# Performance work log

Measured on AMD Instinct MI355X. Metric: run time of the kernel, lower is better.

The kernel has to match this reference:

```python
import jax, jax.numpy as jnp
import numpy as np
import math

# e3nn-style fully-connected Clebsch-Gordan tensor product
# irreps_in1 = 64x0e + 64x1e + 64x2e   (dim 576)
# irreps_in2 =  1x0e +  1x1e +  1x2e   (dim 9, e.g. spherical harmonics)
# irreps_out = 64x0e + 64x1e + 64x2e   (dim 576), shared weights
MUL1, MUL2, MULO = 64, 1, 64
LS = [0, 1, 2]
N_BATCH = 32768


def _su2_cg(j1, m1, j2, m2, j3, m3):
    # SU(2) Clebsch-Gordan coefficient <j1 m1 j2 m2 | j3 m3> (Racah formula)
    if m3 != m1 + m2:
        return 0.0
    f = math.factorial
    c = (2 * j3 + 1) * f(j1 + j2 - j3) * f(j1 - j2 + j3) * f(-j1 + j2 + j3) / f(j1 + j2 + j3 + 1)
    c = math.sqrt(c)
    c *= math.sqrt(f(j3 + m3) * f(j3 - m3) * f(j1 - m1) * f(j1 + m1) * f(j2 - m2) * f(j2 + m2))
    s = 0.0
    for k in range(max(0, j2 - j3 - m1, j1 - j3 + m2), min(j1 + j2 - j3, j1 - m1, j2 + m2) + 1):
        s += (-1.0) ** k / (f(k) * f(j1 + j2 - j3 - k) * f(j1 - m1 - k) * f(j2 + m2 - k)
                            * f(j3 - j2 + m1 + k) * f(j3 - j1 - m2 + k))
    return c * s


def _q_real_to_complex(l):
    # unitary change of basis, columns = real-SH index, rows = complex m (e3nn convention)
    q = np.zeros((2 * l + 1, 2 * l + 1), dtype=np.complex128)
    r2 = 1.0 / math.sqrt(2.0)
    for m in range(-l, 0):
        q[l + m, l + abs(m)] = r2
        q[l + m, l - abs(m)] = -1j * r2
    q[l, l] = 1.0
    for m in range(1, l + 1):
        q[l + m, l + m] = (-1) ** m * r2
        q[l + m, l - m] = 1j * (-1) ** m * r2
    return (-1j) ** l * q


def _real_cg(l1, l2, l3):
    # CG tensor in the real spherical-harmonic basis, unit Frobenius norm (wigner_3j-like)
    C = np.zeros((2 * l1 + 1, 2 * l2 + 1, 2 * l3 + 1), dtype=np.complex128)
    for m1 in range(-l1, l1 + 1):
        for m2 in range(-l2, l2 + 1):
            m3 = m1 + m2
            if abs(m3) <= l3:
                C[l1 + m1, l2 + m2, l3 + m3] = _su2_cg(l1, m1, l2, m2, l3, m3)
    U1, U2, U3 = _q_real_to_complex(l1), _q_real_to_complex(l2), _q_real_to_complex(l3)
    Cr = np.einsum('ia,jb,kc,ijk->abc', U1, U2, np.conj(U3), C)
    assert np.abs(Cr.imag).max() < 1e-9, 'real-basis CG should be real'
    Cr = Cr.real
    return (Cr / np.linalg.norm(Cr)).astype(np.float32)


PATHS = [(l1, l2, l3) for l1 in LS for l2 in LS for l3 in LS if abs(l1 - l2) <= l3 <= l1 + l2]
CG = {p: jnp.asarray(_real_cg(*p)) for p in PATHS}
N_PATHS_TO = {l3: sum(1 for p in PATHS if p[2] == l3) for l3 in LS}
ALPHA = {l3: 1.0 / math.sqrt(MUL1 * MUL2 * N_PATHS_TO[l3]) for l3 in LS}  # path normalization
WEIGHT_NUMEL = len(PATHS) * MUL1 * MUL2 * MULO  # 15 * 4096 = 61440
DIM1 = MUL1 * sum(2 * l + 1 for l in LS)  # 576
DIM2 = MUL2 * sum(2 * l + 1 for l in LS)  # 9


def _split1(x):
    segs, off = [], 0
    for l in LS:
        d = MUL1 * (2 * l + 1)
        segs.append(x[:, off:off + d].reshape(-1, MUL1, 2 * l + 1))
        off += d
    return segs


def _split2(y):
    segs, off = [], 0
    for l in LS:
        d = 2 * l + 1
        segs.append(y[:, off:off + d])
        off += d
    return segs


def tensor_product(x, y, W):
    # W (x (CG-otimes) y): per-path weighted Clebsch-Gordan contraction
    xs, ys = _split1(x), _split2(y)  # xs[l]: [N,64,2l+1], ys[l]: [N,2l+1]
    N = x.shape[0]
    outs = [jnp.zeros((N, MULO, 2 * l + 1), x.dtype) for l in LS]
    off = 0
    for (l1, l2, l3) in PATHS:
        Wp = W[off:off + MUL1 * MULO].reshape(MUL1, MULO)  # [u, w] (v = 1)
        off += MUL1 * MULO
        outs[l3] = outs[l3] + ALPHA[l3] * jnp.einsum(
            'nui,nj,ijk,uw->nwk', xs[l1], ys[l2], CG[(l1, l2, l3)], Wp)
    return jnp.concatenate([o.reshape(N, -1) for o in outs], axis=-1)  # [N, 576]


def setup_inputs() -> dict:
    key = jax.random.key(0)
    kx, ky, kw = jax.random.split(key, 3)
    x = jax.random.normal(kx, (N_BATCH, DIM1), dtype=jnp.float32)
    y = jax.random.normal(ky, (N_BATCH, DIM2), dtype=jnp.float32)
    W = jax.random.normal(kw, (WEIGHT_NUMEL,), dtype=jnp.float32)
    return {'x': x, 'y': y, 'W': W}


def reference(x, y, W):
    return tensor_product(x, y, W)
```

## Files before the change

### kernel.cpp

```cpp
#include <hip/hip_runtime.h>
#include <cmath>
#include <complex>
#include <algorithm>

#define NPATH 15
constexpr int PL1[NPATH] = {0,0,0, 1,1,1,1,1,1, 2,2,2,2,2,2};
constexpr int PL2[NPATH] = {0,1,2, 0,1,1,1,2,2, 0,1,1,2,2,2};
constexpr int PL3[NPATH] = {0,1,2, 1,0,1,2,1,2, 2,1,2,0,1,2};
constexpr int CGOFF[NPATH] = {0,1,10,35,44,53,80,125,170,245,270,315,390,415,490};
constexpr int CGTOT = 615;
constexpr int YOFF[3] = {0,1,4};

constexpr int GB[8] = {0,9,24,33,48,63,88,103};
constexpr int YGTOT = 137;

struct CGArg { float v[CGTOT]; };

static double factd(int n){ double r=1.0; for(int i=2;i<=n;++i) r*=(double)i; return r; }

static double su2_cg(int j1,int m1,int j2,int m2,int j3,int m3){
  if (m3 != m1+m2) return 0.0;
  double c = (double)(2*j3+1) * factd(j1+j2-j3) * factd(j1-j2+j3) * factd(-j1+j2+j3)
             / factd(j1+j2+j3+1);
  c = std::sqrt(c);
  c *= std::sqrt(factd(j3+m3)*factd(j3-m3)*factd(j1-m1)*factd(j1+m1)*factd(j2-m2)*factd(j2+m2));
  double s = 0.0;
  int kmin = std::max(0, std::max(j2-j3-m1, j1-j3+m2));
  int kmax = std::min(j1+j2-j3, std::min(j1-m1, j2+m2));
  for (int k=kmin;k<=kmax;++k){
    double d = factd(k)*factd(j1+j2-j3-k)*factd(j1-m1-k)*factd(j2+m2-k)
             * factd(j3-j2+m1+k)*factd(j3-j1-m2+k);
    s += ((k&1)? -1.0 : 1.0)/d;
  }
  return c*s;
}

static void qmat(int l, std::complex<double>* q){
  int d = 2*l+1;
  for (int a=0;a<d*d;++a) q[a] = std::complex<double>(0.0,0.0);
  const double r2 = 1.0/std::sqrt(2.0);
  for (int m=-l; m<0; ++m){
    q[(l+m)*d + (l-m)] = std::complex<double>(r2, 0.0);
    q[(l+m)*d + (l+m)] = std::complex<double>(0.0, -r2);
  }
  q[l*d + l] = std::complex<double>(1.0,0.0);
  for (int m=1; m<=l; ++m){
    double sg = (m&1)? -1.0 : 1.0;
    q[(l+m)*d + (l+m)] = std::complex<double>(sg*r2, 0.0);
    q[(l+m)*d + (l-m)] = std::complex<double>(0.0, sg*r2);
  }
  std::complex<double> ph = (l==0)? std::complex<double>(1,0)
                        : (l==1)? std::complex<double>(0,-1)
                                : std::complex<double>(-1,0);
  for (int a=0;a<d*d;++a) q[a] *= ph;
}

static void compute_cg(float* outv){
  const int npaths_to[3] = {3,6,6};
  for (int p=0;p<NPATH;++p){
    int l1=PL1[p], l2=PL2[p], l3=PL3[p];
    int d1=2*l1+1, d2=2*l2+1, d3=2*l3+1;
    std::complex<double> C[5][5][5];
    for (int a=0;a<5;++a) for(int b=0;b<5;++b) for(int c=0;c<5;++c) C[a][b][c]=std::complex<double>(0,0);
    for (int m1=-l1;m1<=l1;++m1) for (int m2=-l2;m2<=l2;++m2){
      int m3=m1+m2;
      if (std::abs(m3)<=l3) C[l1+m1][l2+m2][l3+m3] = su2_cg(l1,m1,l2,m2,l3,m3);
    }
    std::complex<double> U1[25],U2[25],U3[25];
    qmat(l1,U1); qmat(l2,U2); qmat(l3,U3);
    double Cr[5][5][5]; double nrm=0.0;
    for (int a=0;a<d1;++a) for (int b=0;b<d2;++b) for (int c=0;c<d3;++c){
      std::complex<double> s(0,0);
      for (int i=0;i<d1;++i) for (int j=0;j<d2;++j) for (int k=0;k<d3;++k)
        s += U1[i*d1+a]*U2[j*d2+b]*std::conj(U3[k*d3+c])*C[i][j][k];
      Cr[a][b][c] = s.real();
      nrm += s.real()*s.real();
    }
    nrm = std::sqrt(nrm);
    double alpha = 1.0/std::sqrt(64.0*(double)npaths_to[l3]);
    float* o = outv + CGOFF[p];
    int idx=0;
    for (int a=0;a<d1;++a) for (int b=0;b<d2;++b) for (int c=0;c<d3;++c)
      o[idx++] = (float)(Cr[a][b][c]/nrm*alpha);
  }
}

typedef short bf16x8 __attribute__((ext_vector_type(8)));
typedef float f32x4 __attribute__((ext_vector_type(4)));

#define MFMA16(A,B,C) __builtin_amdgcn_mfma_f32_16x16x32_bf16((A),(B),(C),0,0,0)

__device__ __forceinline__ unsigned cvtpk_bf16(float a, float b){
  unsigned r;
  asm("v_cvt_pk_bf16_f32 %0, %1, %2" : "=v"(r) : "v"(a), "v"(b));
  return r;
}

__device__ __forceinline__ bf16x8 afrag(const unsigned short* s_xt, int plane, int kt, int row, int q){
  int c = (kt*4 + q) ^ (row & 7);
  return *reinterpret_cast<const bf16x8*>(s_xt + (plane*16 + row)*64 + c*8);
}
__device__ __forceinline__ bf16x8 wfrag(const unsigned short* WT, int p, int wt, int cl, int kt, int q){
  return *reinterpret_cast<const bf16x8*>(WT + p*4096 + (wt*16+cl)*64 + kt*32 + q*8);
}
__device__ __forceinline__ void xt_write_pk(unsigned short* s_xt, int plane, int n, int t16, uint2 pk){
  const int swz = (((t16>>1)^(n&7))<<3) + ((t16&1)<<2);
  *reinterpret_cast<uint2*>(s_xt + (plane*16 + n)*64 + swz) = pk;
}

__device__ __forceinline__ void pack_x(const float4& r0, const float4* r1, const float4* r2, uint2* xpk){
  const float* f0 = reinterpret_cast<const float*>(&r0);
  const float* f1 = reinterpret_cast<const float*>(r1);
  const float* f2 = reinterpret_cast<const float*>(r2);
  xpk[0].x = cvtpk_bf16(f0[0], f0[1]);  xpk[0].y = cvtpk_bf16(f0[2], f0[3]);
  #pragma unroll
  for (int i=0;i<3;++i){
    xpk[1+i].x = cvtpk_bf16(f1[0*3+i], f1[1*3+i]);
    xpk[1+i].y = cvtpk_bf16(f1[2*3+i], f1[3*3+i]);
  }
  #pragma unroll
  for (int i=0;i<5;++i){
    xpk[4+i].x = cvtpk_bf16(f2[0*5+i], f2[1*5+i]);
    xpk[4+i].y = cvtpk_bf16(f2[2*5+i], f2[3*5+i]);
  }
}

template<int G,int D1,int D3,int AB>
__device__ __forceinline__ void gen1(const bf16x8* xf, bf16x8 b0, bf16x8 b1,
                                     const float* ygc, f32x4* acc){
  const f32x4 z4 = {0.f,0.f,0.f,0.f};
  #pragma unroll
  for (int i=0;i<D1;++i){
    f32x4 T = MFMA16(b0, xf[2*i], z4);  T = MFMA16(b1, xf[2*i+1], T);
    #pragma unroll
    for (int k=0;k<D3;++k){
      float yv = ygc[(GB[G] + i*D3 + k)*16];
      acc[AB+k] += T*yv;
    }
  }
}
template<int D1,int AB>
__device__ __forceinline__ void dl0(const bf16x8* xf, bf16x8 b0, bf16x8 b1,
                                    float cy, f32x4* acc){
  const f32x4 z4 = {0.f,0.f,0.f,0.f};
  #pragma unroll
  for (int i=0;i<D1;++i){
    f32x4 T = MFMA16(b0, xf[2*i], z4);  T = MFMA16(b1, xf[2*i+1], T);
    acc[AB+i] += T*cy;
  }
}
template<int D3,int YE,int AB>
__device__ __forceinline__ void d0l(const bf16x8* xf, bf16x8 b0, bf16x8 b1,
                                    float c, const float* ygc, f32x4* acc){
  const f32x4 z4 = {0.f,0.f,0.f,0.f};
  f32x4 T = MFMA16(b0, xf[0], z4);  T = MFMA16(b1, xf[1], T);
  #pragma unroll
  for (int k=0;k<D3;++k){
    float yv = c*ygc[(YE+k)*16];
    acc[AB+k] += T*yv;
  }
}
template<int D1,int YE>
__device__ __forceinline__ void dll0(const bf16x8* xf, bf16x8 b0, bf16x8 b1,
                                     float c, const float* ygc, f32x4* acc){
  const f32x4 z4 = {0.f,0.f,0.f,0.f};
  f32x4 s = z4;
  #pragma unroll
  for (int i=0;i<D1;++i){
    f32x4 T = MFMA16(b0, xf[2*i], z4);  T = MFMA16(b1, xf[2*i+1], T);
    s += T*ygc[(YE+i)*16];
  }
  acc[0] += s*c;
}

__global__ __launch_bounds__(256, 3)
void tp_kernel(const float* __restrict__ x, const float* __restrict__ y,
               const unsigned short* __restrict__ WT, float* __restrict__ out, CGArg cga)
{
  __shared__ __align__(16) unsigned short s_xt[9*16*64];
  __shared__ __align__(16) float s_yg[YGTOT*16];

  const int bid = blockIdx.x;
  const int tile = (bid & 7) | ((bid >> 4) << 3);
  const int half = (bid >> 3) & 1;
  const int n0 = tile * 16;

  const int tid = threadIdx.x;
  const int n_s = tid>>4, t16 = tid&15;

  {
    const float* xb = x + (size_t)(n0 + n_s)*576;
    float4 r0 = *reinterpret_cast<const float4*>(xb + t16*4);
    float4 r1[3], r2[5];
    #pragma unroll
    for (int i=0;i<3;++i) r1[i] = *reinterpret_cast<const float4*>(xb + 64 + t16*12 + 4*i);
    #pragma unroll
    for (int i=0;i<5;++i) r2[i] = *reinterpret_cast<const float4*>(xb + 256 + t16*20 + 4*i);

    float yl[9];
    {
      const float* yrow = y + (size_t)(n0 + t16)*9;
      #pragma unroll
      for (int j=0;j<9;++j) yl[j] = yrow[j];
    }

    uint2 xpk[9];
    pack_x(r0, r1, r2, xpk);
    #pragma unroll
    for (int pl=0; pl<9; ++pl) xt_write_pk(s_xt, pl, n_s, t16, xpk[pl]);

    if (tid < 16){
      #pragma unroll
      for (int j=0;j<9;++j) s_yg[(128+j)*16 + tid] = yl[j];
    }

    if (half == 0){
      constexpr int GL[4] = {0,2,4,6};
      #pragma unroll
      for (int u=0; u<4; ++u){
        constexpr int GPp[4] = {5,7,10,13};
        const int p = GPp[u];
        const int d2=2*PL2[p]+1, d3=2*PL3[p]+1;
        const int cnt = (2*PL1[p]+1)*d3*16;
        for (int idx=tid; idx<cnt; idx+=256){
          int ik = idx >> 4;
          int i  = ik/d3;
          int k  = ik - i*d3;
          float s=0.f;
          for (int j=0;j<d2;++j)
            s += yl[YOFF[PL2[p]]+j]*cga.v[CGOFF[p]+(i*d2+j)*d3+k];
          s_yg[(GB[GL[u]]+ik)*16 + t16] = s;
        }
      }
    } else {
      constexpr int GL[4] = {1,3,5,7};
      #pragma unroll
      for (int u=0; u<4; ++u){
        constexpr int GPp[4] = {6,8,11,14};
        const int p = GPp[u];
        const int d2=2*PL2[p]+1, d3=2*PL3[p]+1;
        const int cnt = (2*PL1[p]+1)*d3*16;
        for (int idx=tid; idx<cnt; idx+=256){
          int ik = idx >> 4;
          int i  = ik/d3;
          int k  = ik - i*d3;
          float s=0.f;
          for (int j=0;j<d2;++j)
            s += yl[YOFF[PL2[p]]+j]*cga.v[CGOFF[p]+(i*d2+j)*d3+k];
          s_yg[(GB[GL[u]]+ik)*16 + t16] = s;
        }
      }
    }
  }
  __syncthreads();

  const int lane = tid & 63, wt = tid >> 6;
  const int cl = lane & 15, q = lane >> 4;
  const float* ygc = s_yg + cl;
  const float y0 = ygc[128*16];
  const int wbase = wt*16 + q*4;

  const f32x4 z4 = {0.f,0.f,0.f,0.f};
  bf16x8 b0,b1,nb0,nb1;

  #define LDB(P) { nb0 = wfrag(WT,P,wt,cl,0,q); nb1 = wfrag(WT,P,wt,cl,1,q); }
  #define ADV    { b0 = nb0; b1 = nb1; }

  if (half == 0){
    f32x4 acc[4] = {z4,z4,z4,z4};
    bf16x8 xf0[2];
    #pragma unroll
    for (int kt=0;kt<2;++kt) xf0[kt] = afrag(s_xt, 0, kt, cl, q);
    b0 = wfrag(WT,0,wt,cl,0,q); b1 = wfrag(WT,0,wt,cl,1,q);

    LDB(1);  dl0<1,0>(xf0, b0,b1, cga.v[CGOFF[0]]*y0, acc);              ADV;
    LDB(3);  d0l<3,129,1>(xf0, b0,b1, cga.v[CGOFF[1]], ygc, acc);        ADV;
    bf16x8 xf1[6];
    #pragma unroll
    for (int i=0;i<3;++i)
      #pragma unroll
      for (int kt=0;kt<2;++kt) xf1[2*i+kt] = afrag(s_xt, 1+i, kt, cl, q);
    LDB(4);  dl0<3,1>(xf1, b0,b1, cga.v[CGOFF[3]]*y0, acc);              ADV;
    LDB(5);  dll0<3,129>(xf1, b0,b1, cga.v[CGOFF[4]], ygc, acc);         ADV;
    LDB(7);  gen1<0,3,3,1>(xf1, b0,b1, ygc, acc);                        ADV;
    LDB(10); gen1<2,3,3,1>(xf1, b0,b1, ygc, acc);                        ADV;
    bf16x8 xf2[10];
    #pragma unroll
    for (int i=0;i<5;++i)
      #pragma unroll
      for (int kt=0;kt<2;++kt) xf2[2*i+kt] = afrag(s_xt, 4+i, kt, cl, q);
    LDB(12); gen1<4,5,3,1>(xf2, b0,b1, ygc, acc);                        ADV;
    LDB(13); dll0<5,132>(xf2, b0,b1, cga.v[CGOFF[12]], ygc, acc);        ADV;
             gen1<6,5,3,1>(xf2, b0,b1, ygc, acc);

    float* orow = out + (size_t)(n0 + cl)*576;
    *reinterpret_cast<float4*>(orow + wbase) =
        make_float4(acc[0][0],acc[0][1],acc[0][2],acc[0][3]);
    float4 v0 = make_float4(acc[1][0],acc[2][0],acc[3][0],acc[1][1]);
    float4 v1 = make_float4(acc[2][1],acc[3][1],acc[1][2],acc[2][2]);
    float4 v2 = make_float4(acc[3][2],acc[1][3],acc[2][3],acc[3][3]);
    float4* qp = reinterpret_cast<float4*>(orow + 64 + wbase*3);
    qp[0]=v0; qp[1]=v1; qp[2]=v2;
  } else {
    f32x4 acc[5] = {z4,z4,z4,z4,z4};
    bf16x8 xf0[2];
    #pragma unroll
    for (int kt=0;kt<2;++kt) xf0[kt] = afrag(s_xt, 0, kt, cl, q);
    b0 = wfrag(WT,2,wt,cl,0,q); b1 = wfrag(WT,2,wt,cl,1,q);

    LDB(6);  d0l<5,132,0>(xf0, b0,b1, cga.v[CGOFF[2]], ygc, acc);        ADV;
    bf16x8 xf1[6];
    #pragma unroll
    for (int i=0;i<3;++i)
      #pragma unroll
      for (int kt=0;kt<2;++kt) xf1[2*i+kt] = afrag(s_xt, 1+i, kt, cl, q);
    LDB(8);  gen1<1,3,5,0>(xf1, b0,b1, ygc, acc);                        ADV;
    LDB(9);  gen1<3,3,5,0>(xf1, b0,b1, ygc, acc);                        ADV;
    bf16x8 xf2[10];
    #pragma unroll
    for (int i=0;i<5;++i)
      #pragma unroll
      for (int kt=0;kt<2;++kt) xf2[2*i+kt] = afrag(s_xt, 4+i, kt, cl, q);
    LDB(11); dl0<5,0>(xf2, b0,b1, cga.v[CGOFF[9]]*y0, acc);              ADV;
    LDB(14); gen1<5,5,5,0>(xf2, b0,b1, ygc, acc);                        ADV;
             gen1<7,5,5,0>(xf2, b0,b1, ygc, acc);

    float* orow = out + (size_t)(n0 + cl)*576;
    float4 v0 = make_float4(acc[0][0],acc[1][0],acc[2][0],acc[3][0]);
    float4 v1 = make_float4(acc[4][0],acc[0][1],acc[1][1],acc[2][1]);
    float4 v2 = make_float4(acc[3][1],acc[4][1],acc[0][2],acc[1][2]);
    float4 v3 = make_float4(acc[2][2],acc[3][2],acc[4][2],acc[0][3]);
    float4 v4 = make_float4(acc[1][3],acc[2][3],acc[3][3],acc[4][3]);
    float4* qp = reinterpret_cast<float4*>(orow + 256 + wbase*5);
    qp[0]=v0; qp[1]=v1; qp[2]=v2; qp[3]=v3; qp[4]=v4;
  }
  #undef LDB
  #undef ADV
}

__global__ void wt_kernel(const float* __restrict__ W, unsigned short* __restrict__ WT){
  int t = blockIdx.x*256 + threadIdx.x;
  int p = t >> 12, r = t & 4095, w = r >> 6, u = r & 63;
  float f = W[(p<<12) + (u<<6) + w];
  unsigned fu = __builtin_bit_cast(unsigned, f);
  unsigned rr = (fu + 0x7FFFu + ((fu>>16)&1u)) >> 16;
  WT[t] = (unsigned short)rr;
}

extern "C" void kernel_launch(void* const* d_in, const int* in_sizes, int n_in,
                              void* d_out, int out_size, void* d_ws, size_t ws_size,
                              hipStream_t stream) {
  const float* x = (const float*)d_in[0];
  const float* y = (const float*)d_in[1];
  const float* W = (const float*)d_in[2];
  float* out = (float*)d_out;
  (void)in_sizes; (void)n_in; (void)out_size; (void)ws_size;

  unsigned short* WT = (unsigned short*)d_ws;

  CGArg cga;
  compute_cg(cga.v);

  hipLaunchKernelGGL(wt_kernel, dim3(240), dim3(256), 0, stream, W, WT);
  hipLaunchKernelGGL(tp_kernel, dim3(4096), dim3(256), 0, stream, x, y, WT, out, cga);
}
```

Measured before the change: 63.19 us.

## Merge the two half-blocks per tile into one 512-thread block sharing staged x

New measurement: 66.76 us. 1.06x slower.

```diff
diff --git a/kernel.cpp b/kernel.cpp
--- a/kernel.cpp
+++ b/kernel.cpp
@@ -108,23 +108,6 @@
   *reinterpret_cast<uint2*>(s_xt + (plane*16 + n)*64 + swz) = pk;
 }
 
-__device__ __forceinline__ void pack_x(const float4& r0, const float4* r1, const float4* r2, uint2* xpk){
-  const float* f0 = reinterpret_cast<const float*>(&r0);
-  const float* f1 = reinterpret_cast<const float*>(r1);
-  const float* f2 = reinterpret_cast<const float*>(r2);
-  xpk[0].x = cvtpk_bf16(f0[0], f0[1]);  xpk[0].y = cvtpk_bf16(f0[2], f0[3]);
-  #pragma unroll
-  for (int i=0;i<3;++i){
-    xpk[1+i].x = cvtpk_bf16(f1[0*3+i], f1[1*3+i]);
-    xpk[1+i].y = cvtpk_bf16(f1[2*3+i], f1[3*3+i]);
-  }
-  #pragma unroll
-  for (int i=0;i<5;++i){
-    xpk[4+i].x = cvtpk_bf16(f2[0*5+i], f2[1*5+i]);
-    xpk[4+i].y = cvtpk_bf16(f2[2*5+i], f2[3*5+i]);
-  }
-}
-
 template<int G,int D1,int D3,int AB>
 __device__ __forceinline__ void gen1(const bf16x8* xf, bf16x8 b0, bf16x8 b1,
                                      const float* ygc, f32x4* acc){
@@ -173,29 +156,48 @@
   acc[0] += s*c;
 }
 
-__global__ __launch_bounds__(256, 3)
+__global__ __launch_bounds__(512, 4)
 void tp_kernel(const float* __restrict__ x, const float* __restrict__ y,
                const unsigned short* __restrict__ WT, float* __restrict__ out, CGArg cga)
 {
   __shared__ __align__(16) unsigned short s_xt[9*16*64];
   __shared__ __align__(16) float s_yg[YGTOT*16];
 
-  const int bid = blockIdx.x;
-  const int tile = (bid & 7) | ((bid >> 4) << 3);
-  const int half = (bid >> 3) & 1;
-  const int n0 = tile * 16;
-
   const int tid = threadIdx.x;
-  const int n_s = tid>>4, t16 = tid&15;
+  const int n0 = blockIdx.x * 16;
+  const int n_s = (tid>>4)&15, t16 = tid&15, g = tid>>8;
 
   {
     const float* xb = x + (size_t)(n0 + n_s)*576;
-    float4 r0 = *reinterpret_cast<const float4*>(xb + t16*4);
-    float4 r1[3], r2[5];
-    #pragma unroll
-    for (int i=0;i<3;++i) r1[i] = *reinterpret_cast<const float4*>(xb + 64 + t16*12 + 4*i);
-    #pragma unroll
-    for (int i=0;i<5;++i) r2[i] = *reinterpret_cast<const float4*>(xb + 256 + t16*20 + 4*i);
+    if (g==0){
+      float4 r0 = *reinterpret_cast<const float4*>(xb + t16*4);
+      float4 r1[3];
+      #pragma unroll
+      for (int i=0;i<3;++i) r1[i] = *reinterpret_cast<const float4*>(xb + 64 + t16*12 + 4*i);
+      const float* f0 = reinterpret_cast<const float*>(&r0);
+      const float* f1 = reinterpret_cast<const float*>(r1);
+      uint2 pk;
+      pk.x = cvtpk_bf16(f0[0], f0[1]);  pk.y = cvtpk_bf16(f0[2], f0[3]);
+      xt_write_pk(s_xt, 0, n_s, t16, pk);
+      #pragma unroll
+      for (int i=0;i<3;++i){
+        pk.x = cvtpk_bf16(f1[0*3+i], f1[1*3+i]);
+        pk.y = cvtpk_bf16(f1[2*3+i], f1[3*3+i]);
+        xt_write_pk(s_xt, 1+i, n_s, t16, pk);
+      }
+    } else {
+      float4 r2[5];
+      #pragma unroll
+      for (int i=0;i<5;++i) r2[i] = *reinterpret_cast<const float4*>(xb + 256 + t16*20 + 4*i);
+      const float* f2 = reinterpret_cast<const float*>(r2);
+      #pragma unroll
+      for (int i=0;i<5;++i){
+        uint2 pk;
+        pk.x = cvtpk_bf16(f2[0*5+i], f2[1*5+i]);
+        pk.y = cvtpk_bf16(f2[2*5+i], f2[3*5+i]);
+        xt_write_pk(s_xt, 4+i, n_s, t16, pk);
+      }
+    }
 
     float yl[9];
     {
@@ -203,59 +205,32 @@
       #pragma unroll
       for (int j=0;j<9;++j) yl[j] = yrow[j];
     }
-
-    uint2 xpk[9];
-    pack_x(r0, r1, r2, xpk);
-    #pragma unroll
-    for (int pl=0; pl<9; ++pl) xt_write_pk(s_xt, pl, n_s, t16, xpk[pl]);
-
     if (tid < 16){
       #pragma unroll
       for (int j=0;j<9;++j) s_yg[(128+j)*16 + tid] = yl[j];
     }
-
-    if (half == 0){
-      constexpr int GL[4] = {0,2,4,6};
-      #pragma unroll
-      for (int u=0; u<4; ++u){
-        constexpr int GPp[4] = {5,7,10,13};
-        const int p = GPp[u];
-        const int d2=2*PL2[p]+1, d3=2*PL3[p]+1;
-        const int cnt = (2*PL1[p]+1)*d3*16;
-        for (int idx=tid; idx<cnt; idx+=256){
-          int ik = idx >> 4;
-          int i  = ik/d3;
-          int k  = ik - i*d3;
-          float s=0.f;
-          for (int j=0;j<d2;++j)
-            s += yl[YOFF[PL2[p]]+j]*cga.v[CGOFF[p]+(i*d2+j)*d3+k];
-          s_yg[(GB[GL[u]]+ik)*16 + t16] = s;
-        }
+    #pragma unroll
+    for (int gg=0; gg<8; ++gg){
+      constexpr int GPp[8] = {5,6,7,8,10,11,13,14};
+      const int p = GPp[gg];
+      const int d2=2*PL2[p]+1, d3=2*PL3[p]+1;
+      const int cnt = (2*PL1[p]+1)*d3*16;
+      for (int idx=tid; idx<cnt; idx+=512){
+        int ik = idx >> 4;
+        int i  = ik/d3;
+        int k  = ik - i*d3;
+        float s=0.f;
+        for (int j=0;j<d2;++j)
+          s += yl[YOFF[PL2[p]]+j]*cga.v[CGOFF[p]+(i*d2+j)*d3+k];
+        s_yg[(GB[gg]+ik)*16 + t16] = s;
       }
-    } else {
-      constexpr int GL[4] = {1,3,5,7};
-      #pragma unroll
-      for (int u=0; u<4; ++u){
-        constexpr int GPp[4] = {6,8,11,14};
-        const int p = GPp[u];
-        const int d2=2*PL2[p]+1, d3=2*PL3[p]+1;
-        const int cnt = (2*PL1[p]+1)*d3*16;
-        for (int idx=tid; idx<cnt; idx+=256){
-          int ik = idx >> 4;
-          int i  = ik/d3;
-          int k  = ik - i*d3;
-          float s=0.f;
-          for (int j=0;j<d2;++j)
-            s += yl[YOFF[PL2[p]]+j]*cga.v[CGOFF[p]+(i*d2+j)*d3+k];
-          s_yg[(GB[GL[u]]+ik)*16 + t16] = s;
-        }
-      }
     }
   }
   __syncthreads();
 
-  const int lane = tid & 63, wt = tid >> 6;
+  const int lane = tid & 63, wid = tid >> 6;
   const int cl = lane & 15, q = lane >> 4;
+  const int wt = wid & 3, half = wid >> 2;
   const float* ygc = s_yg + cl;
   const float y0 = ygc[128*16];
   const int wbase = wt*16 + q*4;
@@ -362,5 +337,5 @@
   compute_cg(cga.v);
 
   hipLaunchKernelGGL(wt_kernel, dim3(240), dim3(256), 0, stream, W, WT);
-  hipLaunchKernelGGL(tp_kernel, dim3(4096), dim3(256), 0, stream, x, y, WT, out, cga);
-}
+  hipLaunchKernelGGL(tp_kernel, dim3(2048), dim3(512), 0, stream, x, y, WT, out, cga);
+}
```
